# Performance work log

Hardware: AMD Instinct MI355X
Metric: run time of the kernel (lower is better)

Reference implementation:

```python
import jax, jax.numpy as jnp
import numpy as np

V, B, NT, EN, EMB, ODIM = 5000, 512, 50, 200, 200, 40
PERP = 30.0
BETA_TEMP = 0.2
SINKHORN_ALPHA = 20.0
WEIGHT_ECR = 250.0
ECR_ITERS = 100
SNE_ITERS = 20
EPS_DIV = 1e-16


def _pairwise_sq(x, y):
    # ||x_i||^2 + ||y_j||^2 - 2 x_i . y_j  (matches module's pairwise_euclidean_distance)
    return (jnp.sum(x * x, axis=1)[:, None] + jnp.sum(y * y, axis=1)[None, :]
            - 2.0 * (x @ y.T))


def _bn_train(x, g, b):
    # BatchNorm1d, training mode: batch statistics, biased variance
    m = x.mean(axis=0)
    v = x.var(axis=0)
    return (x - m) / jnp.sqrt(v + 1e-5) * g + b


def _snekhorn_reduce(X, proj):
    # SNEkhorn-style symmetric entropic affinity on rows of X (log-domain
    # symmetric Sinkhorn with uniform marginals), followed by a linear readout
    # to ODIM dims. X: (n, d) -> (n, ODIM).
    C = _pairwise_sq(X, X)                       # (n, n)
    n = X.shape[0]
    eps = jnp.mean(C) / jnp.log(PERP) + 1e-6     # bandwidth tied to perplexity
    log_a = -jnp.log(float(n))                   # uniform target marginal

    @jax.checkpoint
    def step(f, _):
        lse = jax.nn.logsumexp((f[None, :] - C) / eps, axis=1)
        f = 0.5 * (f + eps * (log_a - lse))      # symmetric Sinkhorn update
        return f, None

    f, _ = jax.lax.scan(step, jnp.zeros(n, C.dtype), None, length=SNE_ITERS)
    P = jnp.exp((f[:, None] + f[None, :] - C) / eps)  # (n, n) affinity
    return P @ proj                                   # (n, ODIM)


def _ecr_loss(cost):
    # ECR: entropic OT between topic and word embeddings (fixed-iteration Sinkhorn)
    Km = jnp.exp(-cost * SINKHORN_ALPHA)          # (NT, V)
    a = jnp.full((NT, 1), 1.0 / NT, cost.dtype)
    bm = jnp.full((V, 1), 1.0 / V, cost.dtype)

    def step(u, _):
        v = bm / (Km.T @ u + EPS_DIV)
        u = a / (Km @ v + EPS_DIV)
        return u, None

    u, _ = jax.lax.scan(step, jnp.full((NT, 1), 1.0 / NT, cost.dtype), None,
                        length=ECR_ITERS)
    v = bm / (Km.T @ u + EPS_DIV)
    transp = u * (Km * v.T)
    return WEIGHT_ECR * jnp.sum(transp * cost)


def setup_inputs() -> dict:
    key = jax.random.key(0)
    ks = jax.random.split(key, 12)

    def nrm(k, shape, s=0.02):
        return jax.random.normal(k, shape, jnp.float32) * s

    word_emb = jax.random.normal(ks[0], (V, EMB), jnp.float32)
    word_emb = word_emb / jnp.linalg.norm(word_emb, axis=1, keepdims=True)
    topic_emb = jax.random.normal(ks[1], (NT, EMB), jnp.float32) * 0.1
    topic_emb = topic_emb / jnp.linalg.norm(topic_emb, axis=1, keepdims=True)

    return dict(
        bow=jax.random.uniform(ks[2], (B, V), jnp.float32),
        eps_noise=jax.random.normal(ks[3], (ODIM, NT), jnp.float32),
        W1=nrm(ks[4], (EN, V)), b1=jnp.zeros(EN, jnp.float32),
        W2=nrm(ks[5], (EN, EN)), b2=jnp.zeros(EN, jnp.float32),
        Wmu=nrm(ks[6], (NT, EN)), bmu=jnp.zeros(NT, jnp.float32),
        Wlv=nrm(ks[7], (NT, EN)), blv=jnp.zeros(NT, jnp.float32),
        g_mu=jnp.ones(NT, jnp.float32), be_mu=jnp.zeros(NT, jnp.float32),
        g_lv=jnp.ones(NT, jnp.float32), be_lv=jnp.zeros(NT, jnp.float32),
        g_dec=jnp.ones(V, jnp.float32), be_dec=jnp.zeros(V, jnp.float32),
        word_emb=word_emb, topic_emb=topic_emb,
        proj_V=nrm(ks[8], (V, ODIM), 1.0),
        proj_K=nrm(ks[9], (NT, ODIM), 1.0),
    )


def reference(bow, eps_noise, W1, b1, W2, b2, Wmu, bmu, Wlv, blv,
              g_mu, be_mu, g_lv, be_lv, g_dec, be_dec,
              word_emb, topic_emb, proj_V, proj_K):
    # bow_reduced = SNEkhorn(bow.T).T : (ODIM, V)
    bow_reduced = _snekhorn_reduce(bow.T, proj_V).T

    # encoder1: Linear -> softplus -> Linear -> softplus
    e1 = jax.nn.softplus(bow_reduced @ W1.T + b1)
    e1 = jax.nn.softplus(e1 @ W2.T + b2)
    mu = _bn_train(e1 @ Wmu.T + bmu, g_mu, be_mu)        # (ODIM, NT)
    logvar = _bn_train(e1 @ Wlv.T + blv, g_lv, be_lv)

    z = mu + eps_noise * jnp.exp(0.5 * logvar)           # reparameterize (training)
    theta = jax.nn.softmax(z, axis=1)                    # (ODIM, NT)
    theta_reduced = _snekhorn_reduce(theta.T, proj_K).T  # (ODIM, NT)

    # KL vs logistic-normal prior; with a = ones: mu2 = 0, var2 = 1 - 1/NT
    var2 = 1.0 - 1.0 / NT
    var = jnp.exp(logvar)
    kld = 0.5 * ((var / var2 + mu * mu / var2 + jnp.log(var2) - logvar).sum(axis=1) - NT)
    loss_KL = kld.mean()

    # beta + decode (cost computed once; torch code computes it twice identically)
    cost = _pairwise_sq(topic_emb, word_emb)             # (NT, V)
    beta = jax.nn.softmax(-cost / BETA_TEMP, axis=0)
    recon = jax.nn.softmax(_bn_train(theta_reduced @ beta, g_dec, be_dec), axis=-1)
    recon_loss = -(bow_reduced * jnp.log(recon)).sum(axis=1).mean()

    loss_TM = recon_loss + loss_KL
    loss_ECR = _ecr_loss(cost)
    loss = loss_TM + loss_ECR
    return loss, loss_TM, loss_ECR, theta_reduced
```

## Files before the change

kernel.cpp:

```cpp
#include <hip/hip_runtime.h>
#include <hip/hip_bf16.h>
#include <hip/hip_fp16.h>

#define VV 5000
#define NTOP 50
#define ENH 200
#define NEMB 200
#define OD 40
#define MP 5120
#define KNS 5008

typedef __attribute__((ext_vector_type(8))) short short8;
typedef __attribute__((ext_vector_type(4))) float f32x4;

constexpr size_t OFF_R      = 0;
constexpr size_t OFF_S      = 20224;
constexpr size_t OFF_SCAL   = 22528;
constexpr size_t OFF_PHIA   = 22784;
constexpr size_t OFF_PHIB   = 43008;
constexpr size_t OFF_ROWS   = 63232;
constexpr size_t OFF_PARTS  = 63744;
constexpr size_t OFF_FLAGS  = 71936;
constexpr size_t OFF_MUPRE  = 72960;
constexpr size_t OFF_LVPRE  = 81152;
constexpr size_t OFF_E1T    = 89344;
constexpr size_t OFF_E2T    = 121600;
constexpr size_t OFF_THRED  = 153856;
constexpr size_t OFF_BOWRED = 162048;
constexpr size_t ZERO_BYTES = 962304;
constexpr size_t OFF_PVT    = 962304;
constexpr size_t OFF_XB     = 1453824;
constexpr size_t OFF_CE     = 6696704;
constexpr size_t OFF_COST   = 56696832;
constexpr size_t OFF_KM     = 57697024;
constexpr size_t OFF_BETA   = 58697216;
constexpr size_t OFF_RN     = 59697408;

__global__ __launch_bounds__(256) void k1_stats(const float* __restrict__ bow,
    __hip_bfloat16* __restrict__ Xb, float* __restrict__ r, float* __restrict__ s){
  __shared__ float lds[64][129];
  const int t = threadIdx.x;
  const int i0 = blockIdx.x * 128, d0 = blockIdx.y * 64;
  #pragma unroll
  for (int m = 0; m < 32; ++m){
    int idx = m*256 + t;
    int di = idx >> 7;
    int ii = idx & 127;
    int gi = i0 + ii;
    lds[di][ii] = (gi < VV) ? bow[(size_t)(d0+di)*VV + gi] : 0.f;
  }
  __syncthreads();
  if (t < 128 && (i0 + t) < VV){
    float acc = 0.f;
    for (int di = 0; di < 64; ++di){ float v = lds[di][t]; acc += v*v; }
    atomicAdd(&r[i0+t], acc);
  }
  if (t < 64){
    float acc = 0.f;
    for (int ii = 0; ii < 128; ++ii) acc += lds[t][ii];
    atomicAdd(&s[d0+t], acc);
  }
  __syncthreads();
  #pragma unroll
  for (int m = 0; m < 32; ++m){
    int idx = m*256 + t;
    int ii = idx >> 6;
    int dd = idx & 63;
    Xb[(size_t)(i0+ii)*512 + d0 + dd] = __float2bfloat16(lds[dd][ii]);
  }
}

__global__ __launch_bounds__(256) void k2_eps(const float* __restrict__ r,
    const float* __restrict__ s, float* __restrict__ scal){
  const int t = threadIdx.x;
  float a = 0.f, b = 0.f;
  for (int i = t; i < VV; i += 256) a += r[i];
  for (int d = t; d < 512; d += 256){ float v = s[d]; b += v*v; }
  #pragma unroll
  for (int off = 32; off; off >>= 1){
    a += __shfl_down(a, off, 64);
    b += __shfl_down(b, off, 64);
  }
  __shared__ float ra[4], rb[4];
  int lane = t & 63, w = t >> 6;
  if (lane == 0){ ra[w] = a; rb[w] = b; }
  __syncthreads();
  if (t == 0){
    float sa = ra[0]+ra[1]+ra[2]+ra[3];
    float sb = rb[0]+rb[1]+rb[2]+rb[3];
    float meanC = 2.f*sa/(float)VV - 2.f*sb/((float)VV*(float)VV);
    float eps = meanC / logf(30.f) + 1e-6f;
    scal[0] = eps;
    scal[1] = 1.f/eps;
  }
}

__device__ __forceinline__ void ecr_block(int b, int it_base, int n_iters, bool do_final,
    const __half* __restrict__ Kn, const float* __restrict__ cost,
    float* __restrict__ acc, int* __restrict__ cnt, float* __restrict__ scal,
    char* smem){
  __half* KmL = (__half*)smem;
  float* varr = (float*)(smem + 32208);
  float* us   = (float*)(smem + 33488);
  float* p5   = (float*)(smem + 33696);
  float* redr = (float*)(smem + 34736);
  const int t = threadIdx.x;
  const int base = (b < 8) ? b*313 : 2504 + (b-8)*312;
  const int sz   = (b < 8) ? 313 : 312;
  for (int c = t; c < 322; c += 256){
    if (c < sz){
      #pragma unroll
      for (int q = 0; q < NTOP; ++q)
        KmL[q*322 + c] = Kn[(size_t)q*KNS + base + c];
    } else {
      #pragma unroll
      for (int q = 0; q < NTOP; ++q) KmL[q*322 + c] = __float2half(0.f);
    }
  }
  if (t < 52){
    float u0 = 0.f;
    if (t < NTOP){
      if (it_base == 0) u0 = 1.f/(float)NTOP;
      else {
        float sm = __hip_atomic_load(&acc[((it_base-1)%3)*64 + t],
                                     __ATOMIC_RELAXED, __HIP_MEMORY_SCOPE_AGENT);
        u0 = (1.f/(float)NTOP)/(sm + 1e-16f);
      }
    }
    us[t] = u0;
  }
  for (int c = sz + t; c < 320; c += 256) varr[c] = 0.f;
  __syncthreads();
  const bool act = (2*t < sz);
  for (int k = 0; k < n_iters; ++k){
    const int g = it_base + k;
    if (act){
      float w0 = 0.f, w1 = 0.f, w2 = 0.f, w3 = 0.f;
      #pragma unroll
      for (int q = 0; q < NTOP; q += 2){
        float u0 = us[q], u1 = us[q+1];
        float2 f0 = __half22float2(*(const __half2*)(KmL + q*322 + 2*t));
        float2 f1 = __half22float2(*(const __half2*)(KmL + (q+1)*322 + 2*t));
        w0 += f0.x*u0; w1 += f0.y*u0;
        w2 += f1.x*u1; w3 += f1.y*u1;
      }
      float2 vv;
      vv.x = (1.f/(float)VV)/((w0+w2) + 1e-16f);
      vv.y = (2*t+1 < sz) ? (1.f/(float)VV)/((w1+w3) + 1e-16f) : 0.f;
      *(float2*)(varr + 2*t) = vv;
    }
    __syncthreads();
    if (t < 250){
      const int qq = t % NTOP, stripe = t / NTOP;
      const __half* kp = KmL + qq*322 + stripe*64;
      const float* vp = varr + stripe*64;
      float s0 = 0.f, s1 = 0.f, s2 = 0.f, s3 = 0.f;
      #pragma unroll
      for (int n = 0; n < 64; n += 4){
        float2 fa = __half22float2(*(const __half2*)(kp + n));
        float2 fb = __half22float2(*(const __half2*)(kp + n + 2));
        float4 v4 = *(const float4*)(vp + n);
        s0 += fa.x*v4.x; s1 += fa.y*v4.y; s2 += fb.x*v4.z; s3 += fb.y*v4.w;
      }
      p5[stripe*52 + qq] = (s0+s1)+(s2+s3);
    }
    __syncthreads();
    if (t < NTOP){
      float sm = p5[t] + p5[52+t] + p5[104+t] + p5[156+t] + p5[208+t];
      __hip_atomic_fetch_add(&acc[(g%3)*64 + t], sm,
                             __ATOMIC_RELAXED, __HIP_MEMORY_SCOPE_AGENT);
    }
    __asm__ volatile("s_waitcnt vmcnt(0)" ::: "memory");
    if (t == 0){
      __hip_atomic_fetch_add(cnt, 1, __ATOMIC_RELEASE, __HIP_MEMORY_SCOPE_AGENT);
      const int tgt = 16*(g+1);
      while (__hip_atomic_load(cnt, __ATOMIC_ACQUIRE, __HIP_MEMORY_SCOPE_AGENT) < tgt)
        __builtin_amdgcn_s_sleep(1);
    }
    if (t < NTOP){
      float sm = __hip_atomic_load(&acc[(g%3)*64 + t],
                                   __ATOMIC_RELAXED, __HIP_MEMORY_SCOPE_AGENT);
      us[t] = (1.f/(float)NTOP)/(sm + 1e-16f);
    }
    if (t < 64)
      __hip_atomic_store(&acc[((g+2)%3)*64 + t], 0.f,
                         __ATOMIC_RELAXED, __HIP_MEMORY_SCOPE_AGENT);
    __syncthreads();
  }
  if (!do_final) return;
  float lsum = 0.f;
  if (act){
    float w0 = 0.f, w1 = 0.f, w2 = 0.f, w3 = 0.f;
    #pragma unroll
    for (int q = 0; q < NTOP; q += 2){
      float u0 = us[q], u1 = us[q+1];
      float2 f0 = __half22float2(*(const __half2*)(KmL + q*322 + 2*t));
      float2 f1 = __half22float2(*(const __half2*)(KmL + (q+1)*322 + 2*t));
      w0 += f0.x*u0; w1 += f0.y*u0;
      w2 += f1.x*u1; w3 += f1.y*u1;
    }
    float v0 = (1.f/(float)VV)/((w0+w2) + 1e-16f);
    const bool ok1 = (2*t+1 < sz);
    float v1 = ok1 ? (1.f/(float)VV)/((w1+w3) + 1e-16f) : 0.f;
    float accv = 0.f;
    #pragma unroll
    for (int q = 0; q < NTOP; ++q){
      float2 f = __half22float2(*(const __half2*)(KmL + q*322 + 2*t));
      float uq = us[q];
      float c0 = cost[(size_t)q*VV + base + 2*t];
      accv += uq*f.x*v0*c0;
      if (ok1){
        float c1 = cost[(size_t)q*VV + base + 2*t + 1];
        accv += uq*f.y*v1*c1;
      }
    }
    lsum = accv;
  }
  #pragma unroll
  for (int off = 32; off; off >>= 1) lsum += __shfl_down(lsum, off, 64);
  if ((t & 63) == 0) redr[t >> 6] = lsum;
  __syncthreads();
  if (t == 0) atomicAdd(&scal[3], redr[0]+redr[1]+redr[2]+redr[3]);
}

__global__ __launch_bounds__(256) void k3_gemm_ecr(const __hip_bfloat16* __restrict__ Xb,
    const float* __restrict__ r, float* __restrict__ scal, __half* __restrict__ Ce,
    const __half* __restrict__ Kn, const float* __restrict__ cost,
    float* __restrict__ accg, int* __restrict__ cnt){
  __shared__ __align__(16) char smem[36864];
  if (blockIdx.x < 16){
    ecr_block(blockIdx.x, 0, 20, false, Kn, cost, accg, cnt, scal, smem);
    return;
  }
  __hip_bfloat16* As = (__hip_bfloat16*)smem;
  __hip_bfloat16* Bs = (__hip_bfloat16*)(smem + 128*72*2);
  const int b2 = blockIdx.x - 16;
  const int t = threadIdx.x;
  const int i0 = (b2 % 40) * 128, j0 = (b2 / 40) * 128;
  const int lane = t & 63, w = t >> 6;
  const int wr = w >> 1, wc = w & 1;
  const int m16 = lane & 15, q4 = lane >> 4;
  f32x4 acc[4][4];
  #pragma unroll
  for (int a = 0; a < 4; ++a)
    #pragma unroll
    for (int b = 0; b < 4; ++b) acc[a][b] = (f32x4){0.f,0.f,0.f,0.f};
  const int srow = t >> 3, sseg = t & 7;
  for (int kc = 0; kc < 512; kc += 64){
    __syncthreads();
    #pragma unroll
    for (int m = 0; m < 4; ++m){
      int row = m*32 + srow;
      uint4 va = *(const uint4*)(Xb + (size_t)(i0+row)*512 + kc + sseg*8);
      *(uint4*)(As + row*72 + sseg*8) = va;
      uint4 vb = *(const uint4*)(Xb + (size_t)(j0+row)*512 + kc + sseg*8);
      *(uint4*)(Bs + row*72 + sseg*8) = vb;
    }
    __syncthreads();
    #pragma unroll
    for (int ks = 0; ks < 64; ks += 32){
      short8 af[4], bf[4];
      #pragma unroll
      for (int f = 0; f < 4; ++f){
        af[f] = *(const short8*)(As + (wr*64 + f*16 + m16)*72 + ks + q4*8);
        bf[f] = *(const short8*)(Bs + (wc*64 + f*16 + m16)*72 + ks + q4*8);
      }
      #pragma unroll
      for (int fr = 0; fr < 4; ++fr)
        #pragma unroll
        for (int fc = 0; fc < 4; ++fc)
          acc[fr][fc] = __builtin_amdgcn_mfma_f32_16x16x32_bf16(af[fr], bf[fc], acc[fr][fc], 0, 0, 0);
    }
  }
  const float inv_eps = scal[1];
  #pragma unroll
  for (int fr = 0; fr < 4; ++fr){
    int rbase = i0 + wr*64 + fr*16 + q4*4;
    #pragma unroll
    for (int fc = 0; fc < 4; ++fc){
      int col = j0 + wc*64 + fc*16 + m16;
      if (col < VV){
        float rc = r[col];
        #pragma unroll
        for (int q = 0; q < 4; ++q){
          int row = rbase + q;
          if (row < VV){
            float val = (r[row] + rc - 2.f*acc[fr][fc][q]) * inv_eps;
            Ce[(size_t)row*VV + col] = __float2half(val);
          }
        }
      }
    }
  }
}

__global__ __launch_bounds__(256) void k4_sweep_ecr(const __half* __restrict__ Ce,
    const float* __restrict__ phi_in, float* __restrict__ phi_out,
    const __half* __restrict__ Kn, const float* __restrict__ cost,
    float* __restrict__ accg, int* __restrict__ cnt, float* __restrict__ scal,
    int it_base){
  __shared__ __align__(16) char smem[34752];
  const int t = threadIdx.x;
  if (blockIdx.x < 16){
    ecr_block(blockIdx.x, it_base, 4, it_base + 4 == 100, Kn, cost, accg, cnt, scal, smem);
    return;
  }
  const int i0 = (blockIdx.x - 16) * 8;
  float acc[8];
  #pragma unroll
  for (int rr = 0; rr < 8; ++rr) acc[rr] = 0.f;
  for (int c = t; c < 2500; c += 256){
    float2 ph = ((const float2*)phi_in)[c];
    #pragma unroll
    for (int rr = 0; rr < 8; ++rr){
      __half2 h2 = *((const __half2*)(Ce + (size_t)(i0+rr)*VV) + c);
      float2 ce = __half22float2(h2);
      acc[rr] += __expf(ph.x - ce.x) + __expf(ph.y - ce.y);
    }
  }
  #pragma unroll
  for (int rr = 0; rr < 8; ++rr)
    #pragma unroll
    for (int off = 32; off; off >>= 1)
      acc[rr] += __shfl_down(acc[rr], off, 64);
  float* red = (float*)smem;
  int lane = t & 63, w = t >> 6;
  if (lane == 0){
    #pragma unroll
    for (int rr = 0; rr < 8; ++rr) red[w*8 + rr] = acc[rr];
  }
  __syncthreads();
  if (t < 8){
    float ssum = red[t] + red[8+t] + red[16+t] + red[24+t];
    const float loga = -8.517193191416238f;
    float lse = __logf(ssum);
    phi_out[i0 + t] = 0.5f*(phi_in[i0 + t] + loga - lse);
  }
}

__global__ __launch_bounds__(256) void k5p_pvt(const float* __restrict__ projV,
    __hip_bfloat16* __restrict__ pvt){
  int idx = blockIdx.x*256 + threadIdx.x;
  if (idx >= 48*MP) return;
  int n = idx / MP, j = idx - n*MP;
  float v = (n < OD && j < VV) ? projV[(size_t)j*OD + n] : 0.f;
  pvt[idx] = __float2bfloat16(v);
}

__global__ __launch_bounds__(256) void k5_bowred(const __half* __restrict__ Ce,
    const float* __restrict__ phi, const __hip_bfloat16* __restrict__ pvt,
    float* __restrict__ brpA, float* __restrict__ brpB){
  __shared__ __align__(16) char smem[25600];
  __hip_bfloat16* As = (__hip_bfloat16*)smem;
  __hip_bfloat16* Bs = (__hip_bfloat16*)(smem + 18432);
  const int t = threadIdx.x;
  const int i0 = blockIdx.x * 128;
  const int k0 = blockIdx.y * 640;
  const int lane = t & 63, w = t >> 6;
  const int m16 = lane & 15, q4 = lane >> 4;
  f32x4 acc[2][3];
  #pragma unroll
  for (int a = 0; a < 2; ++a)
    #pragma unroll
    for (int b = 0; b < 3; ++b) acc[a][b] = (f32x4){0.f,0.f,0.f,0.f};
  for (int kc = k0; kc < k0 + 640; kc += 64){
    __syncthreads();
    #pragma unroll
    for (int m = 0; m < 4; ++m){
      int g = m*256 + t;
      int row = g >> 3, cg = g & 7;
      int gi = i0 + row, j2 = kc + cg*8;
      union { __hip_bfloat16 h[8]; short8 v; } u;
      if (gi < VV && j2 < VV){
        uint4 vce = *(const uint4*)(Ce + (size_t)gi*VV + j2);
        const __half2* hp = (const __half2*)&vce;
        float pb = phi[gi];
        float4 pj0 = *(const float4*)(phi + j2);
        float4 pj1 = *(const float4*)(phi + j2 + 4);
        float pj[8] = {pj0.x,pj0.y,pj0.z,pj0.w,pj1.x,pj1.y,pj1.z,pj1.w};
        #pragma unroll
        for (int e = 0; e < 4; ++e){
          float2 ce = __half22float2(hp[e]);
          u.h[2*e]   = __float2bfloat16(__expf(pb + pj[2*e]   - ce.x));
          u.h[2*e+1] = __float2bfloat16(__expf(pb + pj[2*e+1] - ce.y));
        }
      } else {
        #pragma unroll
        for (int e = 0; e < 8; ++e) u.h[e] = __float2bfloat16(0.f);
      }
      *(short8*)(As + row*72 + cg*8) = u.v;
    }
    #pragma unroll
    for (int m = 0; m < 12; ++m){
      int idx = m*256 + t;
      int row = idx >> 6, c = idx & 63;
      Bs[row*72 + c] = pvt[(size_t)row*MP + kc + c];
    }
    __syncthreads();
    #pragma unroll
    for (int ks = 0; ks < 64; ks += 32){
      short8 af[2], bf[3];
      #pragma unroll
      for (int f = 0; f < 2; ++f)
        af[f] = *(const short8*)(As + (w*32 + f*16 + m16)*72 + ks + q4*8);
      #pragma unroll
      for (int f = 0; f < 3; ++f)
        bf[f] = *(const short8*)(Bs + (f*16 + m16)*72 + ks + q4*8);
      #pragma unroll
      for (int fr = 0; fr < 2; ++fr)
        #pragma unroll
        for (int fc = 0; fc < 3; ++fc)
          acc[fr][fc] = __builtin_amdgcn_mfma_f32_16x16x32_bf16(af[fr], bf[fc], acc[fr][fc], 0, 0, 0);
    }
  }
  __syncthreads();
  float* LF = (float*)smem;
  #pragma unroll
  for (int fr = 0; fr < 2; ++fr){
    int lr = w*32 + fr*16 + q4*4;
    #pragma unroll
    for (int fc = 0; fc < 3; ++fc){
      int col = fc*16 + m16;
      #pragma unroll
      for (int q = 0; q < 4; ++q)
        LF[col*133 + lr + q] = acc[fr][fc][q];
    }
  }
  __syncthreads();
  float* brp = (blockIdx.y < 6) ? brpA + (size_t)blockIdx.y*200000
                                : brpB + (size_t)(blockIdx.y - 6)*200000;
  for (int o = t; o < OD*128; o += 256){
    int col = o >> 7, row = o & 127;
    int gr = i0 + row;
    if (gr < VV) brp[(size_t)col*VV + gr] = LF[col*133 + row];
  }
}

__global__ __launch_bounds__(256) void k5r_red(const float* __restrict__ brpA,
    const float* __restrict__ brpB, float* __restrict__ br){
  int idx = blockIdx.x*256 + threadIdx.x;
  if (idx >= 50000) return;
  const float4* a = (const float4*)brpA;
  const float4* b = (const float4*)brpB;
  float4 s = a[idx];
  #pragma unroll
  for (int sl = 1; sl < 6; ++sl){
    float4 v = a[(size_t)sl*50000 + idx];
    s.x += v.x; s.y += v.y; s.z += v.z; s.w += v.w;
  }
  #pragma unroll
  for (int sl = 0; sl < 2; ++sl){
    float4 v = b[(size_t)sl*50000 + idx];
    s.x += v.x; s.y += v.y; s.z += v.z; s.w += v.w;
  }
  ((float4*)br)[idx] = s;
}

__global__ __launch_bounds__(256) void k6_e1(const float* __restrict__ br,
    const float* __restrict__ W1, float* __restrict__ e1pre){
  const int t = threadIdx.x;
  const int lane = t & 63, w = t >> 6;
  const int k = blockIdx.x*4 + w;
  const int f0 = blockIdx.y * 125;
  float acc[OD];
  #pragma unroll
  for (int i = 0; i < OD; ++i) acc[i] = 0.f;
  const float4* w4p = (const float4*)(W1 + (size_t)k*VV);
  for (int f4 = f0 + lane; f4 < f0 + 125; f4 += 64){
    float4 wv = w4p[f4];
    #pragma unroll
    for (int i = 0; i < OD; ++i){
      float4 bv = ((const float4*)(br + (size_t)i*VV))[f4];
      acc[i] += bv.x*wv.x + bv.y*wv.y + bv.z*wv.z + bv.w*wv.w;
    }
  }
  #pragma unroll
  for (int i = 0; i < OD; ++i)
    #pragma unroll
    for (int off = 32; off; off >>= 1)
      acc[i] += __shfl_down(acc[i], off, 64);
  __shared__ float red[4][OD];
  if (lane == 0){
    #pragma unroll
    for (int i = 0; i < OD; ++i) red[w][i] = acc[i];
  }
  __syncthreads();
  if (t < 160){
    int ww = t / OD, i = t - ww*OD;
    int kk = blockIdx.x*4 + ww;
    atomicAdd(&e1pre[kk*OD + i], red[ww][i]);
  }
}

__global__ __launch_bounds__(256) void k6b_sp(const float* __restrict__ b1,
    float* __restrict__ e1t){
// ... 220 lines not shown
        const float4 tv = *(const float4*)(&Tt[d][tg*4]);
        const float4 wv = *(const float4*)(&wed[d][jg*4]);
        am[0][0] += tv.x*wv.x; am[0][1] += tv.x*wv.y; am[0][2] += tv.x*wv.z; am[0][3] += tv.x*wv.w;
        am[1][0] += tv.y*wv.x; am[1][1] += tv.y*wv.y; am[1][2] += tv.y*wv.z; am[1][3] += tv.y*wv.w;
        am[2][0] += tv.z*wv.x; am[2][1] += tv.z*wv.y; am[2][2] += tv.z*wv.z; am[2][3] += tv.z*wv.w;
        am[3][0] += tv.w*wv.x; am[3][1] += tv.w*wv.y; am[3][2] += tv.w*wv.z; am[3][3] += tv.w*wv.w;
      }
    }
  }
  if (t < NTOP) tn[t] = tnp;
  if (t >= 64 && t < 128) wn[t-64] = wnp;
  __syncthreads();
  if (t < 208){
    #pragma unroll
    for (int a = 0; a < 4; ++a){
      int t50 = tg*4 + a;
      if (t50 < NTOP){
        float tv = tn[t50];
        float cc[4];
        #pragma unroll
        for (int b = 0; b < 4; ++b) cc[b] = tv + wn[jg*4+b] - 2.f*am[a][b];
        int gj = j0 + jg*4;
        if (gj + 3 < VV)
          *(float4*)(cost + (size_t)t50*VV + gj) = make_float4(cc[0],cc[1],cc[2],cc[3]);
        #pragma unroll
        for (int b = 0; b < 4; ++b) sc[t50][jg*4+b] = -5.f*cc[b];
      }
    }
  }
  __syncthreads();
  if (t < 64){
    int gj = j0 + t;
    if (gj < VV){
      float mx = -1e30f;
      for (int q = 0; q < NTOP; ++q) mx = fmaxf(mx, sc[q][t]);
      float ssum = 0.f;
      for (int q = 0; q < NTOP; ++q){ float e = __expf(sc[q][t]-mx); sc[q][t] = e; ssum += e; }
      float inv = 1.f/ssum;
      for (int q = 0; q < NTOP; ++q){
        float e = sc[q][t];
        float e2 = e*e;
        Kn[(size_t)q*KNS + gj] = __float2half(e2*e2);
        beta[(size_t)q*VV + gj] = e*inv;
      }
    }
  }
}

__global__ __launch_bounds__(256) void k12_reconA(const float* __restrict__ thred,
    const float* __restrict__ beta, const float* __restrict__ g_dec,
    const float* __restrict__ be_dec, float* __restrict__ Rn){
  __shared__ float trs[OD][NTOP];
  const int t = threadIdx.x;
  for (int o = t; o < OD*NTOP; o += 256) trs[o/NTOP][o - (o/NTOP)*NTOP] = thred[o];
  __syncthreads();
  int j = blockIdx.x*256 + t;
  if (j >= VV) return;
  float a[OD];
  #pragma unroll
  for (int i = 0; i < OD; ++i) a[i] = 0.f;
  for (int q = 0; q < NTOP; ++q){
    float bv = beta[(size_t)q*VV + j];
    #pragma unroll
    for (int i = 0; i < OD; ++i) a[i] += trs[i][q]*bv;
  }
  float m = 0.f;
  #pragma unroll
  for (int i = 0; i < OD; ++i) m += a[i];
  m *= (1.f/OD);
  float v = 0.f;
  #pragma unroll
  for (int i = 0; i < OD; ++i){ float d = a[i]-m; v += d*d; }
  v *= (1.f/OD);
  float scale = g_dec[j]*rsqrtf(v + 1e-5f);
  float sh = be_dec[j];
  #pragma unroll
  for (int i = 0; i < OD; ++i) Rn[(size_t)i*VV + j] = (a[i]-m)*scale + sh;
}

__global__ __launch_bounds__(256) void k13_reconB(const float* __restrict__ Rn,
    const float* __restrict__ br, float* __restrict__ rows){
  const int i = blockIdx.x;
  const int t = threadIdx.x;
  float s1 = 0.f, s2 = 0.f, s3 = 0.f;
  for (int j = t; j < VV; j += 256){
    float rn = Rn[(size_t)i*VV + j];
    float bv = br[(size_t)i*VV + j];
    s1 += __expf(rn);
    s2 += bv*rn;
    s3 += bv;
  }
  #pragma unroll
  for (int off = 32; off; off >>= 1){
    s1 += __shfl_down(s1, off, 64);
    s2 += __shfl_down(s2, off, 64);
    s3 += __shfl_down(s3, off, 64);
  }
  __shared__ float red[3][4];
  int lane = t & 63, w = t >> 6;
  if (lane == 0){ red[0][w] = s1; red[1][w] = s2; red[2][w] = s3; }
  __syncthreads();
  if (t == 0){
    rows[i]      = red[0][0]+red[0][1]+red[0][2]+red[0][3];
    rows[40 + i] = red[1][0]+red[1][1]+red[1][2]+red[1][3];
    rows[80 + i] = red[2][0]+red[2][1]+red[2][2]+red[2][3];
  }
}

__global__ void k14_final(const float* __restrict__ rows, const float* __restrict__ scal,
    float* __restrict__ out){
  const int t = threadIdx.x;
  float v = 0.f;
  if (t < OD) v = rows[40 + t] - logf(rows[t]) * rows[80 + t];
  #pragma unroll
  for (int off = 32; off; off >>= 1) v += __shfl_down(v, off, 64);
  if (t == 0){
    float recon = -v * (1.f/OD);
    float tm = recon + scal[2];
    float ecr = 250.f * scal[3];
    out[0] = tm + ecr;
    out[1] = tm;
    out[2] = ecr;
  }
}

extern "C" void kernel_launch(void* const* d_in, const int* in_sizes, int n_in,
                              void* d_out, int out_size, void* d_ws, size_t ws_size,
                              hipStream_t stream){
  const float* bow   = (const float*)d_in[0];
  const float* epsn  = (const float*)d_in[1];
  const float* W1    = (const float*)d_in[2];
  const float* b1    = (const float*)d_in[3];
  const float* W2    = (const float*)d_in[4];
  const float* b2    = (const float*)d_in[5];
  const float* Wmu   = (const float*)d_in[6];
  const float* bmu   = (const float*)d_in[7];
  const float* Wlv   = (const float*)d_in[8];
  const float* blv   = (const float*)d_in[9];
  const float* g_mu  = (const float*)d_in[10];
  const float* be_mu = (const float*)d_in[11];
  const float* g_lv  = (const float*)d_in[12];
  const float* be_lv = (const float*)d_in[13];
  const float* g_dec = (const float*)d_in[14];
  const float* be_dec= (const float*)d_in[15];
  const float* wemb  = (const float*)d_in[16];
  const float* temb  = (const float*)d_in[17];
  const float* projV = (const float*)d_in[18];
  const float* projK = (const float*)d_in[19];
  char* ws = (char*)d_ws;
  float* r     = (float*)(ws + OFF_R);
  float* s     = (float*)(ws + OFF_S);
  float* scal  = (float*)(ws + OFF_SCAL);
  float* phiA  = (float*)(ws + OFF_PHIA);
  float* phiB  = (float*)(ws + OFF_PHIB);
  float* rows  = (float*)(ws + OFF_ROWS);
  float* accg  = (float*)(ws + OFF_PARTS);
  int*   cnt   = (int*)(ws + OFF_FLAGS);
  float* mupre = (float*)(ws + OFF_MUPRE);
  float* lvpre = (float*)(ws + OFF_LVPRE);
  float* e1t   = (float*)(ws + OFF_E1T);
  float* e2t   = (float*)(ws + OFF_E2T);
  float* thred = (float*)(ws + OFF_THRED);
  float* br    = (float*)(ws + OFF_BOWRED);
  __hip_bfloat16* pvt = (__hip_bfloat16*)(ws + OFF_PVT);
  __hip_bfloat16* Xb  = (__hip_bfloat16*)(ws + OFF_XB);
  __half* Ce   = (__half*)(ws + OFF_CE);
  float* cost  = (float*)(ws + OFF_COST);
  __half* Kn   = (__half*)(ws + OFF_KM);
  float* beta  = (float*)(ws + OFF_BETA);
  float* Rn    = (float*)(ws + OFF_RN);
  float* brpA  = (float*)(ws + OFF_XB);
  float* brpB  = (float*)(ws + OFF_COST);
  float* out   = (float*)d_out;

  hipMemsetAsync(d_ws, 0, ZERO_BYTES, stream);
  k10_cost<<<79, 256, 0, stream>>>(temb, wemb, cost, Kn, beta);
  k1_stats<<<dim3(40, 8), 256, 0, stream>>>(bow, Xb, r, s);
  k2_eps<<<1, 256, 0, stream>>>(r, s, scal);
  k3_gemm_ecr<<<1616, 256, 0, stream>>>(Xb, r, scal, Ce, Kn, cost, accg, cnt);
  {
    float* pin = phiA; float* pout = phiB;
    for (int itr = 0; itr < 20; ++itr){
      k4_sweep_ecr<<<641, 256, 0, stream>>>(Ce, pin, pout, Kn, cost, accg, cnt,
                                            scal, 20 + 4*itr);
      float* tmp = pin; pin = pout; pout = tmp;
    }
  }
  k5p_pvt<<<960, 256, 0, stream>>>(projV, pvt);
  k5_bowred<<<dim3(40, 8), 256, 0, stream>>>(Ce, phiA, pvt, brpA, brpB);
  k5r_red<<<196, 256, 0, stream>>>(brpA, brpB, br);
  k6_e1<<<dim3(50, 10), 256, 0, stream>>>(br, W1, e1t);
  k6b_sp<<<32, 256, 0, stream>>>(b1, e1t);
  k7_e2<<<50, 256, 0, stream>>>(e1t, W2, b2, e2t);
  k8a_mulv<<<8, 256, 0, stream>>>(e2t, Wmu, bmu, Wlv, blv, mupre, lvpre);
  k8b_theta<<<1, 256, 0, stream>>>(mupre, lvpre, g_mu, be_mu, g_lv, be_lv,
                                   epsn, projK, thred, out + 3, scal);
  k12_reconA<<<20, 256, 0, stream>>>(thred, beta, g_dec, be_dec, Rn);
  k13_reconB<<<40, 256, 0, stream>>>(Rn, br, rows);
  k14_final<<<1, 64, 0, stream>>>(rows, scal, out);
}
```

Baseline: 810.4 us.

## Fuse 20 Sinkhorn sweeps into one persistent kernel with symmetric tile reads

Replaces the 20 separate sweep launches with a single persistent kernel of 836 blocks that synchronises across blocks through atomic counters in global memory. Each block handles an upper-triangular 128x128 tile of the symmetric fp16 cost matrix and adds both row and column partial sums, so roughly half of the matrix is read per iteration. The ECR Sinkhorn work now runs all 80 of its iterations inside 16 dedicated blocks of the same launch. This removes launch overhead and halves memory traffic. In exchange it adds atomic accumulation, two grid barriers per iteration, and a dependency on all 836 blocks being co-resident, otherwise the barriers deadlock.

```diff
diff --git a/kernel.cpp b/kernel.cpp
--- a/kernel.cpp
+++ b/kernel.cpp
@@ -294,47 +294,118 @@
   }
 }
 
-__global__ __launch_bounds__(256) void k4_sweep_ecr(const __half* __restrict__ Ce,
-    const float* __restrict__ phi_in, float* __restrict__ phi_out,
+__global__ __launch_bounds__(256, 4) void k4_persist(const __half* __restrict__ Ce,
+    float* __restrict__ phiA, float* __restrict__ phiB,
+    float* __restrict__ ssum, int* __restrict__ scnt,
     const __half* __restrict__ Kn, const float* __restrict__ cost,
-    float* __restrict__ accg, int* __restrict__ cnt, float* __restrict__ scal,
-    int it_base){
+    float* __restrict__ accg, int* __restrict__ cnt, float* __restrict__ scal){
   __shared__ __align__(16) char smem[34752];
   const int t = threadIdx.x;
   if (blockIdx.x < 16){
-    ecr_block(blockIdx.x, it_base, 4, it_base + 4 == 100, Kn, cost, accg, cnt, scal, smem);
+    ecr_block(blockIdx.x, 20, 80, true, Kn, cost, accg, cnt, scal, smem);
     return;
   }
-  const int i0 = (blockIdx.x - 16) * 8;
-  float acc[8];
-  #pragma unroll
-  for (int rr = 0; rr < 8; ++rr) acc[rr] = 0.f;
-  for (int c = t; c < 2500; c += 256){
-    float2 ph = ((const float2*)phi_in)[c];
-    #pragma unroll
-    for (int rr = 0; rr < 8; ++rr){
-      __half2 h2 = *((const __half2*)(Ce + (size_t)(i0+rr)*VV) + c);
-      float2 ce = __half22float2(h2);
-      acc[rr] += __expf(ph.x - ce.x) + __expf(ph.y - ce.y);
-    }
-  }
-  #pragma unroll
-  for (int rr = 0; rr < 8; ++rr)
-    #pragma unroll
-    for (int off = 32; off; off >>= 1)
-      acc[rr] += __shfl_down(acc[rr], off, 64);
-  float* red = (float*)smem;
-  int lane = t & 63, w = t >> 6;
-  if (lane == 0){
-    #pragma unroll
-    for (int rr = 0; rr < 8; ++rr) red[w*8 + rr] = acc[rr];
-  }
-  __syncthreads();
-  if (t < 8){
-    float ssum = red[t] + red[8+t] + red[16+t] + red[24+t];
-    const float loga = -8.517193191416238f;
-    float lse = __logf(ssum);
-    phi_out[i0 + t] = 0.5f*(phi_in[i0 + t] + loga - lse);
+  const int s = blockIdx.x - 16;
+  int bi = 0, rem = s;
+  while (rem >= 40 - bi){ rem -= 40 - bi; ++bi; }
+  const int bj = bi + rem;
+  const int i0 = bi*128, j0 = bj*128;
+  const bool diag = (bi == bj);
+  float* phiI = (float*)smem;
+  float* phiJ = (float*)smem + 128;
+  float* colred = (float*)smem + 256;
+  const int cg = t & 15;
+  const int rw = t >> 4;
+  const int jbase = j0 + cg*8;
+  const bool colok = (jbase + 8 <= VV);
+  const int cls = s & 15;
+  const float loga = -8.517193191416238f;
+  for (int g = 0; g < 20; ++g){
+    const float* pin = (g & 1) ? phiB : phiA;
+    float* pout = (g & 1) ? phiA : phiB;
+    float* scur = ssum + (size_t)(g & 1)*5120;
+    float* snxt = ssum + (size_t)((g + 1) & 1)*5120;
+    if (t < 128){
+      int gi = i0 + t;
+      phiI[t] = (gi < VV) ? __hip_atomic_load(pin + gi, __ATOMIC_RELAXED,
+                                              __HIP_MEMORY_SCOPE_AGENT) : 0.f;
+    } else {
+      int gj = j0 + t - 128;
+      phiJ[t-128] = (gj < VV) ? __hip_atomic_load(pin + gj, __ATOMIC_RELAXED,
+                                                  __HIP_MEMORY_SCOPE_AGENT) : 0.f;
+    }
+    __syncthreads();
+    float pj[8];
+    #pragma unroll
+    for (int e = 0; e < 8; ++e) pj[e] = phiJ[cg*8 + e];
+    float colacc[8];
+    #pragma unroll
+    for (int e = 0; e < 8; ++e) colacc[e] = 0.f;
+    #pragma unroll
+    for (int p = 0; p < 8; ++p){
+      int row = p*16 + rw;
+      int gi = i0 + row;
+      float rsum = 0.f;
+      if (gi < VV && colok){
+        uint4 vce = *(const uint4*)(Ce + (size_t)gi*VV + jbase);
+        const __half2* hp = (const __half2*)&vce;
+        float pi = phiI[row];
+        #pragma unroll
+        for (int e2 = 0; e2 < 4; ++e2){
+          float2 ce2 = __half22float2(hp[e2]);
+          rsum += __expf(pj[2*e2] - ce2.x) + __expf(pj[2*e2+1] - ce2.y);
+          if (!diag){
+            colacc[2*e2]   += __expf(pi - ce2.x);
+            colacc[2*e2+1] += __expf(pi - ce2.y);
+          }
+        }
+      }
+      #pragma unroll
+      for (int off = 8; off; off >>= 1) rsum += __shfl_down(rsum, off, 16);
+      if (cg == 0 && gi < VV) atomicAdd(&scur[gi], rsum);
+    }
+    if (!diag){
+      #pragma unroll
+      for (int e = 0; e < 8; ++e) colred[rw*128 + cg*8 + e] = colacc[e];
+      __syncthreads();
+      if (t < 128){
+        float sm = 0.f;
+        #pragma unroll
+        for (int k2 = 0; k2 < 16; ++k2) sm += colred[k2*128 + t];
+        int gj = j0 + t;
+        if (gj < VV) atomicAdd(&scur[gj], sm);
+      }
+    }
+    __syncthreads();
+    if (t == 0)
+      __hip_atomic_fetch_add(&scnt[cls*16], 1, __ATOMIC_RELEASE, __HIP_MEMORY_SCOPE_AGENT);
+    if (t < 16){
+      int tgt = (2*g + 1) * ((t < 4) ? 52 : 51);
+      while (__hip_atomic_load(&scnt[t*16], __ATOMIC_ACQUIRE, __HIP_MEMORY_SCOPE_AGENT) < tgt)
+        __builtin_amdgcn_s_sleep(2);
+    }
+    __syncthreads();
+    if (s < 20){
+      if (t < 250){
+        int i = s*250 + t;
+        float ph = __hip_atomic_load(pin + i, __ATOMIC_RELAXED, __HIP_MEMORY_SCOPE_AGENT);
+        float sm = __hip_atomic_load(&scur[i], __ATOMIC_RELAXED, __HIP_MEMORY_SCOPE_AGENT);
+        float nv = 0.5f*(ph + loga - __logf(sm));
+        __hip_atomic_store(pout + i, nv, __ATOMIC_RELAXED, __HIP_MEMORY_SCOPE_AGENT);
+      }
+    } else if (s < 40){
+      int idx = (s - 20)*256 + t;
+      __hip_atomic_store(&snxt[idx], 0.f, __ATOMIC_RELAXED, __HIP_MEMORY_SCOPE_AGENT);
+    }
+    __syncthreads();
+    if (t == 0)
+      __hip_atomic_fetch_add(&scnt[cls*16], 1, __ATOMIC_RELEASE, __HIP_MEMORY_SCOPE_AGENT);
+    if (t < 16){
+      int tgt = (2*g + 2) * ((t < 4) ? 52 : 51);
+      while (__hip_atomic_load(&scnt[t*16], __ATOMIC_ACQUIRE, __HIP_MEMORY_SCOPE_AGENT) < tgt)
+        __builtin_amdgcn_s_sleep(2);
+    }
+    __syncthreads();
   }
 }
 
@@ -886,21 +957,18 @@
   float* Rn    = (float*)(ws + OFF_RN);
   float* brpA  = (float*)(ws + OFF_XB);
   float* brpB  = (float*)(ws + OFF_COST);
+  float* ssum  = (float*)(ws + OFF_RN);
+  int*   scnt  = (int*)(ws + OFF_RN + 40960);
   float* out   = (float*)d_out;
 
   hipMemsetAsync(d_ws, 0, ZERO_BYTES, stream);
+  hipMemsetAsync(ws + OFF_RN, 0, 41984, stream);
   k10_cost<<<79, 256, 0, stream>>>(temb, wemb, cost, Kn, beta);
   k1_stats<<<dim3(40, 8), 256, 0, stream>>>(bow, Xb, r, s);
   k2_eps<<<1, 256, 0, stream>>>(r, s, scal);
   k3_gemm_ecr<<<1616, 256, 0, stream>>>(Xb, r, scal, Ce, Kn, cost, accg, cnt);
-  {
-    float* pin = phiA; float* pout = phiB;
-    for (int itr = 0; itr < 20; ++itr){
-      k4_sweep_ecr<<<641, 256, 0, stream>>>(Ce, pin, pout, Kn, cost, accg, cnt,
-                                            scal, 20 + 4*itr);
-      float* tmp = pin; pin = pout; pout = tmp;
-    }
-  }
+  k4_persist<<<836, 256, 0, stream>>>(Ce, phiA, phiB, ssum, scnt,
+                                      Kn, cost, accg, cnt, scal);
   k5p_pvt<<<960, 256, 0, stream>>>(projV, pvt);
   k5_bowred<<<dim3(40, 8), 256, 0, stream>>>(Ce, phiA, pvt, brpA, brpB);
   k5r_red<<<196, 256, 0, stream>>>(brpA, brpB, br);
```

Result: slower. 2.651 ms (+227.1%).

## Vectorize Sinkhorn sweep loads, halve rows per block, rebalance ECR iterations

Applied to the files above, without the earlier changes.

The SNEkhorn sweep kernel now processes 4 rows per block instead of 8, doubling the grid to 1266 blocks. Each thread loads 16-byte vectors of eight fp16 cost entries and eight phi values instead of half2 pairs. The ECR Sinkhorn iterations overlapped with these kernels are redistributed: 12 in the GEMM kernel, then 4 or 5 per sweep launch, so the ECR blocks' work better matches the shorter sweep kernels. The aim is more memory-level parallelism and wider loads on the bandwidth-bound sweep, at the cost of more blocks each doing less reduction work.

```diff
diff --git a/kernel.cpp b/kernel.cpp
--- a/kernel.cpp
+++ b/kernel.cpp
@@ -229,7 +229,7 @@
     float* __restrict__ accg, int* __restrict__ cnt){
   __shared__ __align__(16) char smem[36864];
   if (blockIdx.x < 16){
-    ecr_block(blockIdx.x, 0, 20, false, Kn, cost, accg, cnt, scal, smem);
+    ecr_block(blockIdx.x, 0, 12, false, Kn, cost, accg, cnt, scal, smem);
     return;
   }
   __hip_bfloat16* As = (__hip_bfloat16*)smem;
@@ -298,28 +298,36 @@
     const float* __restrict__ phi_in, float* __restrict__ phi_out,
     const __half* __restrict__ Kn, const float* __restrict__ cost,
     float* __restrict__ accg, int* __restrict__ cnt, float* __restrict__ scal,
-    int it_base){
+    int it_base, int n_ecr){
   __shared__ __align__(16) char smem[34752];
   const int t = threadIdx.x;
   if (blockIdx.x < 16){
-    ecr_block(blockIdx.x, it_base, 4, it_base + 4 == 100, Kn, cost, accg, cnt, scal, smem);
+    ecr_block(blockIdx.x, it_base, n_ecr, it_base + n_ecr == 100,
+              Kn, cost, accg, cnt, scal, smem);
     return;
   }
-  const int i0 = (blockIdx.x - 16) * 8;
-  float acc[8];
-  #pragma unroll
-  for (int rr = 0; rr < 8; ++rr) acc[rr] = 0.f;
-  for (int c = t; c < 2500; c += 256){
-    float2 ph = ((const float2*)phi_in)[c];
-    #pragma unroll
-    for (int rr = 0; rr < 8; ++rr){
-      __half2 h2 = *((const __half2*)(Ce + (size_t)(i0+rr)*VV) + c);
-      float2 ce = __half22float2(h2);
-      acc[rr] += __expf(ph.x - ce.x) + __expf(ph.y - ce.y);
-    }
-  }
-  #pragma unroll
-  for (int rr = 0; rr < 8; ++rr)
+  const int i0 = (blockIdx.x - 16) * 4;
+  float acc[4] = {0.f, 0.f, 0.f, 0.f};
+  const uint4* ce0 = (const uint4*)(Ce + (size_t)i0*VV);
+  for (int u = t; u < 625; u += 256){
+    float4 p0 = *(const float4*)(phi_in + u*8);
+    float4 p1 = *(const float4*)(phi_in + u*8 + 4);
+    #pragma unroll
+    for (int rr = 0; rr < 4; ++rr){
+      uint4 v = ce0[(size_t)rr*625 + u];
+      const __half2* hp = (const __half2*)&v;
+      float2 c0 = __half22float2(hp[0]);
+      float2 c1 = __half22float2(hp[1]);
+      float2 c2 = __half22float2(hp[2]);
+      float2 c3 = __half22float2(hp[3]);
+      acc[rr] += __expf(p0.x - c0.x) + __expf(p0.y - c0.y)
+               + __expf(p0.z - c1.x) + __expf(p0.w - c1.y)
+               + __expf(p1.x - c2.x) + __expf(p1.y - c2.y)
+               + __expf(p1.z - c3.x) + __expf(p1.w - c3.y);
+    }
+  }
+  #pragma unroll
+  for (int rr = 0; rr < 4; ++rr)
     #pragma unroll
     for (int off = 32; off; off >>= 1)
       acc[rr] += __shfl_down(acc[rr], off, 64);
@@ -327,14 +335,13 @@
   int lane = t & 63, w = t >> 6;
   if (lane == 0){
     #pragma unroll
-    for (int rr = 0; rr < 8; ++rr) red[w*8 + rr] = acc[rr];
-  }
-  __syncthreads();
-  if (t < 8){
-    float ssum = red[t] + red[8+t] + red[16+t] + red[24+t];
+    for (int rr = 0; rr < 4; ++rr) red[w*4 + rr] = acc[rr];
+  }
+  __syncthreads();
+  if (t < 4){
+    float ssum = red[t] + red[4+t] + red[8+t] + red[12+t];
     const float loga = -8.517193191416238f;
-    float lse = __logf(ssum);
-    phi_out[i0 + t] = 0.5f*(phi_in[i0 + t] + loga - lse);
+    phi_out[i0 + t] = 0.5f*(phi_in[i0 + t] + loga - __logf(ssum));
   }
 }
 
@@ -895,9 +902,12 @@
   k3_gemm_ecr<<<1616, 256, 0, stream>>>(Xb, r, scal, Ce, Kn, cost, accg, cnt);
   {
     float* pin = phiA; float* pout = phiB;
+    int itb = 12;
     for (int itr = 0; itr < 20; ++itr){
-      k4_sweep_ecr<<<641, 256, 0, stream>>>(Ce, pin, pout, Kn, cost, accg, cnt,
-                                            scal, 20 + 4*itr);
+      int n = (itr < 12) ? 4 : 5;
+      k4_sweep_ecr<<<1266, 256, 0, stream>>>(Ce, pin, pout, Kn, cost, accg, cnt,
+                                             scal, itb, n);
+      itb += n;
       float* tmp = pin; pin = pout; pout = tmp;
     }
   }
```

After: 845.8 us. +4.4%, slower.

## Exploit cost-matrix symmetry in SNEkhorn sweep with tile-pair partials and intra-kernel sync

Applied to the files above, without the earlier changes.

Each SNEkhorn iteration now visits only upper-triangular 128x128 tiles of the symmetric half-precision cost matrix. Every tile produces both row and column partial sums of exp(-C) weighted by exp(phi), so the matrix is read about half as often. The per-row partials are reduced and phi is updated inside the next launch, using an atomic counter spin-wait that makes the tile blocks wait for the reducer blocks. The ECR Sinkhorn blocks are spread further, with 8 of their iterations moved into the stats kernel. The risks are deadlock if the reducer blocks are not scheduled before the spinning blocks, and precision loss from factoring exp(phi_j - C) into exp(phi_j)*exp(-C), which can underflow.

```diff
diff --git a/kernel.cpp b/kernel.cpp
--- a/kernel.cpp
+++ b/kernel.cpp
@@ -17,8 +17,9 @@
 constexpr size_t OFF_S      = 20224;
 constexpr size_t OFF_SCAL   = 22528;
 constexpr size_t OFF_PHIA   = 22784;
-constexpr size_t OFF_PHIB   = 43008;
+constexpr size_t OFF_EY     = 43008;
 constexpr size_t OFF_ROWS   = 63232;
+constexpr size_t OFF_RCNT   = 63712;
 constexpr size_t OFF_PARTS  = 63744;
 constexpr size_t OFF_FLAGS  = 71936;
 constexpr size_t OFF_MUPRE  = 72960;
@@ -36,65 +37,6 @@
 constexpr size_t OFF_BETA   = 58697216;
 constexpr size_t OFF_RN     = 59697408;
 
-__global__ __launch_bounds__(256) void k1_stats(const float* __restrict__ bow,
-    __hip_bfloat16* __restrict__ Xb, float* __restrict__ r, float* __restrict__ s){
-  __shared__ float lds[64][129];
-  const int t = threadIdx.x;
-  const int i0 = blockIdx.x * 128, d0 = blockIdx.y * 64;
-  #pragma unroll
-  for (int m = 0; m < 32; ++m){
-    int idx = m*256 + t;
-    int di = idx >> 7;
-    int ii = idx & 127;
-    int gi = i0 + ii;
-    lds[di][ii] = (gi < VV) ? bow[(size_t)(d0+di)*VV + gi] : 0.f;
-  }
-  __syncthreads();
-  if (t < 128 && (i0 + t) < VV){
-    float acc = 0.f;
-    for (int di = 0; di < 64; ++di){ float v = lds[di][t]; acc += v*v; }
-    atomicAdd(&r[i0+t], acc);
-  }
-  if (t < 64){
-    float acc = 0.f;
-    for (int ii = 0; ii < 128; ++ii) acc += lds[t][ii];
-    atomicAdd(&s[d0+t], acc);
-  }
-  __syncthreads();
-  #pragma unroll
-  for (int m = 0; m < 32; ++m){
-    int idx = m*256 + t;
-    int ii = idx >> 6;
-    int dd = idx & 63;
-    Xb[(size_t)(i0+ii)*512 + d0 + dd] = __float2bfloat16(lds[dd][ii]);
-  }
-}
-
-__global__ __launch_bounds__(256) void k2_eps(const float* __restrict__ r,
-    const float* __restrict__ s, float* __restrict__ scal){
-  const int t = threadIdx.x;
-  float a = 0.f, b = 0.f;
-  for (int i = t; i < VV; i += 256) a += r[i];
-  for (int d = t; d < 512; d += 256){ float v = s[d]; b += v*v; }
-  #pragma unroll
-  for (int off = 32; off; off >>= 1){
-    a += __shfl_down(a, off, 64);
-    b += __shfl_down(b, off, 64);
-  }
-  __shared__ float ra[4], rb[4];
-  int lane = t & 63, w = t >> 6;
-  if (lane == 0){ ra[w] = a; rb[w] = b; }
-  __syncthreads();
-  if (t == 0){
-    float sa = ra[0]+ra[1]+ra[2]+ra[3];
-    float sb = rb[0]+rb[1]+rb[2]+rb[3];
-    float meanC = 2.f*sa/(float)VV - 2.f*sb/((float)VV*(float)VV);
-    float eps = meanC / logf(30.f) + 1e-6f;
-    scal[0] = eps;
-    scal[1] = 1.f/eps;
-  }
-}
-
 __device__ __forceinline__ void ecr_block(int b, int it_base, int n_iters, bool do_final,
     const __half* __restrict__ Kn, const float* __restrict__ cost,
     float* __restrict__ acc, int* __restrict__ cnt, float* __restrict__ scal,
@@ -223,13 +165,81 @@
   if (t == 0) atomicAdd(&scal[3], redr[0]+redr[1]+redr[2]+redr[3]);
 }
 
+__global__ __launch_bounds__(256) void k1_stats(const float* __restrict__ bow,
+    __hip_bfloat16* __restrict__ Xb, float* __restrict__ r, float* __restrict__ s,
+    const __half* __restrict__ Kn, const float* __restrict__ cost,
+    float* __restrict__ accg, int* __restrict__ cnt, float* __restrict__ scal){
+  __shared__ __align__(16) char smem[34816];
+  const int t = threadIdx.x;
+  if (blockIdx.x >= 40){
+    int b = (blockIdx.x - 40)*8 + blockIdx.y;
+    ecr_block(b, 0, 8, false, Kn, cost, accg, cnt, scal, smem);
+    return;
+  }
+  float (*lds)[129] = (float(*)[129])smem;
+  const int i0 = blockIdx.x * 128, d0 = blockIdx.y * 64;
+  #pragma unroll
+  for (int m = 0; m < 32; ++m){
+    int idx = m*256 + t;
+    int di = idx >> 7;
+    int ii = idx & 127;
+    int gi = i0 + ii;
+    lds[di][ii] = (gi < VV) ? bow[(size_t)(d0+di)*VV + gi] : 0.f;
+  }
+  __syncthreads();
+  if (t < 128 && (i0 + t) < VV){
+    float acc = 0.f;
+    for (int di = 0; di < 64; ++di){ float v = lds[di][t]; acc += v*v; }
+    atomicAdd(&r[i0+t], acc);
+  }
+  if (t < 64){
+    float acc = 0.f;
+    for (int ii = 0; ii < 128; ++ii) acc += lds[t][ii];
+    atomicAdd(&s[d0+t], acc);
+  }
+  __syncthreads();
+  #pragma unroll
+  for (int m = 0; m < 32; ++m){
+    int idx = m*256 + t;
+    int ii = idx >> 6;
+    int dd = idx & 63;
+    Xb[(size_t)(i0+ii)*512 + d0 + dd] = __float2bfloat16(lds[dd][ii]);
+  }
+}
+
+__global__ __launch_bounds__(256) void k2_eps(const float* __restrict__ r,
+    const float* __restrict__ s, float* __restrict__ scal, float* __restrict__ ey){
+  const int t = threadIdx.x;
+  for (int i = t; i < VV; i += 256) ey[i] = 1.f;
+  float a = 0.f, b = 0.f;
+  for (int i = t; i < VV; i += 256) a += r[i];
+  for (int d = t; d < 512; d += 256){ float v = s[d]; b += v*v; }
+  #pragma unroll
+  for (int off = 32; off; off >>= 1){
+    a += __shfl_down(a, off, 64);
+    b += __shfl_down(b, off, 64);
+  }
+  __shared__ float ra[4], rb[4];
+  int lane = t & 63, w = t >> 6;
+  if (lane == 0){ ra[w] = a; rb[w] = b; }
+  __syncthreads();
+  if (t == 0){
+    float sa = ra[0]+ra[1]+ra[2]+ra[3];
+    float sb = rb[0]+rb[1]+rb[2]+rb[3];
+    float meanC = 2.f*sa/(float)VV - 2.f*sb/((float)VV*(float)VV);
+    float eps = meanC / logf(30.f) + 1e-6f;
+    scal[0] = eps;
+    scal[1] = 1.f/eps;
+  }
+}
+
 __global__ __launch_bounds__(256) void k3_gemm_ecr(const __hip_bfloat16* __restrict__ Xb,
     const float* __restrict__ r, float* __restrict__ scal, __half* __restrict__ Ce,
     const __half* __restrict__ Kn, const float* __restrict__ cost,
     float* __restrict__ accg, int* __restrict__ cnt){
   __shared__ __align__(16) char smem[36864];
   if (blockIdx.x < 16){
-    ecr_block(blockIdx.x, 0, 20, false, Kn, cost, accg, cnt, scal, smem);
+    ecr_block(blockIdx.x, 8, 12, false, Kn, cost, accg, cnt, scal, smem);
     return;
   }
   __hip_bfloat16* As = (__hip_bfloat16*)smem;
@@ -294,53 +304,123 @@
   }
 }
 
-__global__ __launch_bounds__(256) void k4_sweep_ecr(const __half* __restrict__ Ce,
-    const float* __restrict__ phi_in, float* __restrict__ phi_out,
-    const __half* __restrict__ Kn, const float* __restrict__ cost,
-    float* __restrict__ accg, int* __restrict__ cnt, float* __restrict__ scal,
-    int it_base){
-  __shared__ __align__(16) char smem[34752];
-  const int t = threadIdx.x;
+__global__ __launch_bounds__(256, 4) void k4_sym(const __half* __restrict__ Ce,
+    float* __restrict__ phi, float* __restrict__ ey, float* __restrict__ part,
+    int* __restrict__ rcnt, const __half* __restrict__ Kn,
+    const float* __restrict__ cost, float* __restrict__ accg,
+    int* __restrict__ cnt, float* __restrict__ scal, int L, int itb){
+  __shared__ __align__(16) char smem[34816];
+  const int t = threadIdx.x;
+  const float loga = -8.517193191416238f;
   if (blockIdx.x < 16){
-    ecr_block(blockIdx.x, it_base, 4, it_base + 4 == 100, Kn, cost, accg, cnt, scal, smem);
+    ecr_block(blockIdx.x, itb, 4, itb + 4 == 100, Kn, cost, accg, cnt, scal, smem);
     return;
   }
-  const int i0 = (blockIdx.x - 16) * 8;
-  float acc[8];
-  #pragma unroll
-  for (int rr = 0; rr < 8; ++rr) acc[rr] = 0.f;
-  for (int c = t; c < 2500; c += 256){
-    float2 ph = ((const float2*)phi_in)[c];
-    #pragma unroll
-    for (int rr = 0; rr < 8; ++rr){
-      __half2 h2 = *((const __half2*)(Ce + (size_t)(i0+rr)*VV) + c);
-      float2 ce = __half22float2(h2);
-      acc[rr] += __expf(ph.x - ce.x) + __expf(ph.y - ce.y);
-    }
-  }
-  #pragma unroll
-  for (int rr = 0; rr < 8; ++rr)
-    #pragma unroll
-    for (int off = 32; off; off >>= 1)
-      acc[rr] += __shfl_down(acc[rr], off, 64);
-  float* red = (float*)smem;
-  int lane = t & 63, w = t >> 6;
-  if (lane == 0){
-    #pragma unroll
-    for (int rr = 0; rr < 8; ++rr) red[w*8 + rr] = acc[rr];
-  }
-  __syncthreads();
-  if (t < 8){
-    float ssum = red[t] + red[8+t] + red[16+t] + red[24+t];
-    const float loga = -8.517193191416238f;
-    float lse = __logf(ssum);
-    phi_out[i0 + t] = 0.5f*(phi_in[i0 + t] + loga - lse);
+  if (blockIdx.x < 36){
+    const int rid = blockIdx.x - 16;
+    if (L > 0 && t < 250){
+      int i = rid*250 + t;
+      float sm = 0.f;
+      #pragma unroll
+      for (int s2 = 0; s2 < 40; ++s2) sm += part[(size_t)s2*VV + i];
+      float ph = 0.5f*(phi[i] + loga - __logf(sm));
+      __hip_atomic_store(&phi[i], ph, __ATOMIC_RELAXED, __HIP_MEMORY_SCOPE_AGENT);
+      __hip_atomic_store(&ey[i], __expf(ph), __ATOMIC_RELAXED, __HIP_MEMORY_SCOPE_AGENT);
+    }
+    __syncthreads();
+    __asm__ volatile("s_waitcnt vmcnt(0)" ::: "memory");
+    if (t == 0)
+      __hip_atomic_fetch_add(rcnt, 1, __ATOMIC_RELEASE, __HIP_MEMORY_SCOPE_AGENT);
+    return;
+  }
+  int bt = blockIdx.x - 36;
+  int bi = 0, rem = bt;
+  while (rem >= 40 - bi){ rem -= 40 - bi; ++bi; }
+  const int bj = bi + rem;
+  const int i0 = bi*128, j0 = bj*128;
+  if (t == 0){
+    const int tgt = 20*(L+1);
+    while (__hip_atomic_load(rcnt, __ATOMIC_ACQUIRE, __HIP_MEMORY_SCOPE_AGENT) < tgt)
+      __builtin_amdgcn_s_sleep(2);
+  }
+  __syncthreads();
+  float* eyI = (float*)smem;
+  float* eyJ = (float*)smem + 128;
+  float* RL  = (float*)smem + 256;
+  if (t < 128){
+    int gi = i0 + t;
+    eyI[t] = (gi < VV) ? __hip_atomic_load(&ey[gi], __ATOMIC_RELAXED,
+                                           __HIP_MEMORY_SCOPE_AGENT) : 0.f;
+  } else {
+    int gj = j0 + (t - 128);
+    eyJ[t-128] = (gj < VV) ? __hip_atomic_load(&ey[gj], __ATOMIC_RELAXED,
+                                               __HIP_MEMORY_SCOPE_AGENT) : 0.f;
+  }
+  __syncthreads();
+  const int rg = t >> 4, cg = t & 15;
+  const bool colok = (j0 + cg*8) < VV;
+  float eyJv[8];
+  #pragma unroll
+  for (int cc = 0; cc < 8; ++cc) eyJv[cc] = eyJ[cg*8 + cc];
+  float rowacc[8], colacc[8];
+  #pragma unroll
+  for (int x = 0; x < 8; ++x){ rowacc[x] = 0.f; colacc[x] = 0.f; }
+  #pragma unroll
+  for (int rr = 0; rr < 8; ++rr){
+    int rloc = rg*8 + rr;
+    int gi = i0 + rloc;
+    if (gi < VV && colok){
+      uint4 v = *(const uint4*)(Ce + (size_t)gi*VV + j0 + cg*8);
+      const __half2* hp = (const __half2*)&v;
+      float eyIr = eyI[rloc];
+      #pragma unroll
+      for (int e = 0; e < 4; ++e){
+        float2 c = __half22float2(hp[e]);
+        float e0 = __expf(-c.x), e1 = __expf(-c.y);
+        rowacc[rr] += e0*eyJv[2*e] + e1*eyJv[2*e+1];
+        colacc[2*e]   += e0*eyIr;
+        colacc[2*e+1] += e1*eyIr;
+      }
+    }
+  }
+  #pragma unroll
+  for (int rr = 0; rr < 8; ++rr) RL[(rg*8+rr)*17 + cg] = rowacc[rr];
+  __syncthreads();
+  if (t < 128){
+    float sm = 0.f;
+    #pragma unroll
+    for (int c2 = 0; c2 < 16; ++c2) sm += RL[t*17 + c2];
+    int gi = i0 + t;
+    if (gi < VV) part[(size_t)bj*VV + gi] = sm;
+  }
+  __syncthreads();
+  #pragma unroll
+  for (int cc = 0; cc < 8; ++cc) RL[(cg*8+cc)*17 + rg] = colacc[cc];
+  __syncthreads();
+  if (bi != bj && t < 128){
+    float sm = 0.f;
+    #pragma unroll
+    for (int r2 = 0; r2 < 16; ++r2) sm += RL[t*17 + r2];
+    int gj = j0 + t;
+    if (gj < VV) part[(size_t)bi*VV + gj] = sm;
   }
 }
 
 __global__ __launch_bounds__(256) void k5p_pvt(const float* __restrict__ projV,
-    __hip_bfloat16* __restrict__ pvt){
-  int idx = blockIdx.x*256 + threadIdx.x;
+    __hip_bfloat16* __restrict__ pvt, const float* __restrict__ part,
+    float* __restrict__ phi){
+  const int t = threadIdx.x;
+  if (blockIdx.x < 20){
+    if (t < 250){
+      int i = blockIdx.x*250 + t;
+      float sm = 0.f;
+      #pragma unroll
+      for (int s2 = 0; s2 < 40; ++s2) sm += part[(size_t)s2*VV + i];
+      phi[i] = 0.5f*(phi[i] + (-8.517193191416238f) - __logf(sm));
+    }
+    return;
+  }
+  int idx = (blockIdx.x - 20)*256 + t;
   if (idx >= 48*MP) return;
   int n = idx / MP, j = idx - n*MP;
   float v = (n < OD && j < VV) ? projV[(size_t)j*OD + n] : 0.f;
@@ -867,8 +947,9 @@
   float* s     = (float*)(ws + OFF_S);
   float* scal  = (float*)(ws + OFF_SCAL);
   float* phiA  = (float*)(ws + OFF_PHIA);
-  float* phiB  = (float*)(ws + OFF_PHIB);
+  float* ey    = (float*)(ws + OFF_EY);
   float* rows  = (float*)(ws + OFF_ROWS);
+  int*   rcnt  = (int*)(ws + OFF_RCNT);
   float* accg  = (float*)(ws + OFF_PARTS);
   int*   cnt   = (int*)(ws + OFF_FLAGS);
   float* mupre = (float*)(ws + OFF_MUPRE);
@@ -877,6 +958,7 @@
   float* e2t   = (float*)(ws + OFF_E2T);
   float* thred = (float*)(ws + OFF_THRED);
   float* br    = (float*)(ws + OFF_BOWRED);
+  float* part  = (float*)(ws + OFF_BOWRED);
   __hip_bfloat16* pvt = (__hip_bfloat16*)(ws + OFF_PVT);
   __hip_bfloat16* Xb  = (__hip_bfloat16*)(ws + OFF_XB);
   __half* Ce   = (__half*)(ws + OFF_CE);
@@ -890,18 +972,13 @@
 
   hipMemsetAsync(d_ws, 0, ZERO_BYTES, stream);
   k10_cost<<<79, 256, 0, stream>>>(temb, wemb, cost, Kn, beta);
-  k1_stats<<<dim3(40, 8), 256, 0, stream>>>(bow, Xb, r, s);
-  k2_eps<<<1, 256, 0, stream>>>(r, s, scal);
+  k1_stats<<<dim3(42, 8), 256, 0, stream>>>(bow, Xb, r, s, Kn, cost, accg, cnt, scal);
+  k2_eps<<<1, 256, 0, stream>>>(r, s, scal, ey);
   k3_gemm_ecr<<<1616, 256, 0, stream>>>(Xb, r, scal, Ce, Kn, cost, accg, cnt);
-  {
-    float* pin = phiA; float* pout = phiB;
-    for (int itr = 0; itr < 20; ++itr){
-      k4_sweep_ecr<<<641, 256, 0, stream>>>(Ce, pin, pout, Kn, cost, accg, cnt,
-                                            scal, 20 + 4*itr);
-      float* tmp = pin; pin = pout; pout = tmp;
-    }
-  }
-  k5p_pvt<<<960, 256, 0, stream>>>(projV, pvt);
+  for (int L = 0; L < 20; ++L)
+    k4_sym<<<856, 256, 0, stream>>>(Ce, phiA, ey, part, rcnt, Kn, cost,
+                                    accg, cnt, scal, L, 20 + 4*L);
+  k5p_pvt<<<980, 256, 0, stream>>>(projV, pvt, part, phiA);
   k5_bowred<<<dim3(40, 8), 256, 0, stream>>>(Ce, phiA, pvt, brpA, brpB);
   k5r_red<<<196, 256, 0, stream>>>(brpA, brpB, br);
   k6_e1<<<dim3(50, 10), 256, 0, stream>>>(br, W1, e1t);
```

Result: slower. 1.702 ms (+110.0%).
